# Kernel optimization log

Hardware: AMD Instinct MI355X
Metric: run time of the kernel (lower is better)

Reference implementation:

```python
import jax, jax.numpy as jnp
import numpy as np
import math

N_HEADS = 16
EMBED_DIM = 1024
HEAD_DIM = EMBED_DIM // N_HEADS


def setup_inputs() -> dict:
    key = jax.random.key(0)
    k1, k2, k3 = jax.random.split(key, 3)
    bs, seq_len = 2, 2048
    x = jax.random.normal(k1, (bs, seq_len, EMBED_DIM), dtype=jnp.float32)
    # torch Linear weights are [out_features, in_features]
    W_in = jax.random.normal(k2, (3 * EMBED_DIM, EMBED_DIM), dtype=jnp.float32) * (1.0 / math.sqrt(EMBED_DIM))
    W_out = jax.random.normal(k3, (EMBED_DIM, EMBED_DIM), dtype=jnp.float32) * (1.0 / math.sqrt(EMBED_DIM))
    return {"x": x, "W_in": W_in, "W_out": W_out, "casual_mask": 1}


def reference(x, W_in, W_out, casual_mask):
    bs, seq_len, embed_dim = x.shape
    # fused QKV projection: x @ W_in.T -> [bs, seq, 3E]
    qkv = jnp.einsum('bse,fe->bsf', x, W_in)
    q, k, v = jnp.split(qkv, 3, axis=-1)
    # [bs, heads, seq, head_dim]
    def to_heads(t):
        return t.reshape(bs, seq_len, N_HEADS, HEAD_DIM).transpose(0, 2, 1, 3)
    q, k, v = to_heads(q), to_heads(k), to_heads(v)
    score = jnp.einsum('bhqd,bhkd->bhqk', q, k)
    if casual_mask:  # static Python flag
        causal = jnp.triu(jnp.ones((seq_len, seq_len), dtype=bool), k=1)
        score = jnp.where(causal, -jnp.inf, score)
    score = score / jnp.asarray(math.sqrt(HEAD_DIM), dtype=score.dtype)
    attn = jax.nn.softmax(score, axis=-1)
    out = jnp.einsum('bhqk,bhkd->bhqd', attn, v)
    out = out.transpose(0, 2, 1, 3).reshape(bs, seq_len, embed_dim)
    return jnp.einsum('bse,fe->bsf', out, W_out)
```

## Files before the change

### kernel.cpp

```cpp
#include <hip/hip_runtime.h>
#include <stdint.h>

#define SEQ 2048
#define BS 2
#define EMB 1024
#define NH 16
#define HD 64
#define F3 3072

using f32x4 = __attribute__((ext_vector_type(4))) float;
using bf16x8 = __attribute__((ext_vector_type(8))) short;

__device__ __forceinline__ unsigned short f2bf(float f) {
    union { float f; uint32_t u; } v; v.f = f;
    uint32_t u = v.u;
    u = u + 0x7FFFu + ((u >> 16) & 1u);
    return (unsigned short)(u >> 16);
}

__device__ __forceinline__ uint32_t pk_bf16(float a, float b) {
    uint32_t r;
    asm("v_cvt_pk_bf16_f32 %0, %1, %2" : "=v"(r) : "v"(a), "v"(b));
    return r;
}

#define GLOAD_LDS16(g, l) \
    __builtin_amdgcn_global_load_lds((const __attribute__((address_space(1))) void*)(g), \
                                     (__attribute__((address_space(3))) void*)(l), 16, 0, 0)

__global__ void cvt_kernel(const float* __restrict__ in, unsigned short* __restrict__ out, int n4) {
    int i = blockIdx.x * blockDim.x + threadIdx.x;
    if (i < n4) {
        f32x4 v = reinterpret_cast<const f32x4*>(in)[i];
        uint2 o;
        o.x = pk_bf16(v.x, v.y);
        o.y = pk_bf16(v.z, v.w);
        reinterpret_cast<uint2*>(out)[i] = o;
    }
}

template <bool BF16OUT>
__global__ __launch_bounds__(256) void gemm_bt(
    const unsigned short* __restrict__ A,
    const unsigned short* __restrict__ B,
    void* __restrict__ Cv,
    int M, int N, int K, int nbx)
{
    __shared__ unsigned short As[128 * 32];
    __shared__ unsigned short Bs[128 * 32];
    const int tid  = threadIdx.x;
    const int wave = tid >> 6, lane = tid & 63;
    const int wr = wave >> 1, wc = wave & 1;

    const int nwg = gridDim.x;
    const int s = (blockIdx.x & 7) * (nwg >> 3) + (blockIdx.x >> 3);
    const int bx = s % nbx, by = s / nbx;
    const int row0 = by * 128, col0 = bx * 128;

    f32x4 acc[4][4] = {};

    const int srow = wave * 16 + (lane >> 2);
    const int scol = (lane & 3) * 8;

    const unsigned short* gA = A + (size_t)(row0 + srow) * K + scol;
    const unsigned short* gB = B + (size_t)(col0 + srow) * K + scol;
    unsigned short* lA = As + wave * 16 * 32;
    unsigned short* lB = Bs + wave * 16 * 32;

    for (int kb = 0; kb < K; kb += 32) {
        __syncthreads();
        GLOAD_LDS16(gA + kb,                    lA);
        GLOAD_LDS16(gA + (size_t)64 * K + kb,   lA + 64 * 32);
        GLOAD_LDS16(gB + kb,                    lB);
        GLOAD_LDS16(gB + (size_t)64 * K + kb,   lB + 64 * 32);
        asm volatile("s_waitcnt vmcnt(0)" ::: "memory");
        __syncthreads();

        bf16x8 af[4], bfr[4];
#pragma unroll
        for (int mi = 0; mi < 4; mi++)
            af[mi] = *reinterpret_cast<const bf16x8*>(As + (wr * 64 + mi * 16 + (lane & 15)) * 32 + (lane >> 4) * 8);
#pragma unroll
        for (int ni = 0; ni < 4; ni++)
            bfr[ni] = *reinterpret_cast<const bf16x8*>(Bs + (wc * 64 + ni * 16 + (lane & 15)) * 32 + (lane >> 4) * 8);
#pragma unroll
        for (int mi = 0; mi < 4; mi++)
#pragma unroll
            for (int ni = 0; ni < 4; ni++)
                acc[mi][ni] = __builtin_amdgcn_mfma_f32_16x16x32_bf16(af[mi], bfr[ni], acc[mi][ni], 0, 0, 0);
    }

#pragma unroll
    for (int mi = 0; mi < 4; mi++)
#pragma unroll
        for (int ni = 0; ni < 4; ni++)
#pragma unroll
            for (int r = 0; r < 4; r++) {
                int row = row0 + wr * 64 + mi * 16 + (lane >> 4) * 4 + r;
                int col = col0 + wc * 64 + ni * 16 + (lane & 15);
                float v = acc[mi][ni][r];
                if constexpr (BF16OUT)
                    ((unsigned short*)Cv)[(size_t)row * N + col] = f2bf(v);
                else
                    ((float*)Cv)[(size_t)row * N + col] = v;
            }
}

__global__ __launch_bounds__(256) void attn_kernel(
    const unsigned short* __restrict__ qkv,
    unsigned short* __restrict__ ao)
{
    const int idx = blockIdx.x;
    const int qb = 15 - (idx >> 5);
    const int bh = idx & 31;
    const int b = bh >> 4, h = bh & 15;
    const int tid = threadIdx.x, wave = tid >> 6, lane = tid & 63;
    const int c = lane & 15, g = lane >> 4;

    __shared__ unsigned short Ks[64 * 64];
    __shared__ unsigned short Vs[64 * 64];
    __shared__ unsigned short Ps[4][32 * 64];

    const size_t base = (size_t)b * SEQ * F3;
    const int qrow0 = qb * 128 + wave * 32;
    const float SC = 0.18033688011f;

    bf16x8 qf[2][2];
#pragma unroll
    for (int qt = 0; qt < 2; qt++)
#pragma unroll
        for (int sdq = 0; sdq < 2; sdq++) {
            int row = qrow0 + qt * 16 + c;
            int d   = sdq * 32 + g * 8;
            qf[qt][sdq] = *reinterpret_cast<const bf16x8*>(qkv + base + (size_t)row * F3 + h * HD + d);
        }

    f32x4 po[2][4] = {};
    float mR[2], lR[2];
    mR[0] = mR[1] = -1e30f; lR[0] = lR[1] = 0.f;

    const int ktiles = (qb * 128 + 128) >> 6;
    const int ksrow = tid >> 3;
    const int sch   = tid & 7;
    const int krow2 = (tid >> 3) * 2;

    const unsigned short* gK = qkv + base + EMB     + h * HD + sch * 8;
    const unsigned short* gV = qkv + base + 2 * EMB + h * HD + sch * 8;

    bf16x8 kp0 = *reinterpret_cast<const bf16x8*>(gK + (size_t)ksrow * F3);
    bf16x8 kp1 = *reinterpret_cast<const bf16x8*>(gK + (size_t)(32 + ksrow) * F3);
    bf16x8 vp0 = *reinterpret_cast<const bf16x8*>(gV + (size_t)krow2 * F3);
    bf16x8 vp1 = *reinterpret_cast<const bf16x8*>(gV + (size_t)(krow2 + 1) * F3);

    for (int kt_i = 0; kt_i < ktiles; kt_i++) {
        const int kbase = kt_i * 64;
        __syncthreads();
        {
            int off0 = (ksrow * 128 + sch * 16) ^ ((ksrow & 7) << 4);
            *reinterpret_cast<bf16x8*>((char*)Ks + off0) = kp0;
            int r1 = 32 + ksrow;
            int off1 = (r1 * 128 + sch * 16) ^ ((r1 & 7) << 4);
            *reinterpret_cast<bf16x8*>((char*)Ks + off1) = kp1;
        }
#pragma unroll
        for (int j = 0; j < 8; j++) {
            int d = sch * 8 + j;
            int off = (d * 128 + krow2 * 2) ^ ((((d & 7) ^ (d >> 3)) & 7) << 4);
            ushort2 pr; pr.x = (unsigned short)vp0[j]; pr.y = (unsigned short)vp1[j];
            *reinterpret_cast<ushort2*>((char*)Vs + off) = pr;
        }
        __syncthreads();

        if (kt_i + 1 < ktiles) {
            const int nb = kbase + 64;
            kp0 = *reinterpret_cast<const bf16x8*>(gK + (size_t)(nb + ksrow) * F3);
            kp1 = *reinterpret_cast<const bf16x8*>(gK + (size_t)(nb + 32 + ksrow) * F3);
            vp0 = *reinterpret_cast<const bf16x8*>(gV + (size_t)(nb + krow2) * F3);
            vp1 = *reinterpret_cast<const bf16x8*>(gV + (size_t)(nb + krow2 + 1) * F3);
        }

        const bool active = kbase <= qrow0 + 31;
        if (active) {
            f32x4 st[4][2] = {};
#pragma unroll
            for (int dstep = 0; dstep < 2; dstep++) {
                bf16x8 kf[4];
#pragma unroll
                for (int kt = 0; kt < 4; kt++) {
                    int row = kt * 16 + c;
                    int off = (row * 128 + dstep * 64 + g * 16) ^ ((row & 7) << 4);
                    kf[kt] = *reinterpret_cast<const bf16x8*>((char*)Ks + off);
                }
#pragma unroll
                for (int kt = 0; kt < 4; kt++)
#pragma unroll
                    for (int qt = 0; qt < 2; qt++)
                        st[kt][qt] = __builtin_amdgcn_mfma_f32_16x16x32_bf16(kf[kt], qf[qt][dstep], st[kt][qt], 0, 0, 0);
            }

            const bool needmask = (kbase + 63) > qrow0;
#pragma unroll
            for (int qt = 0; qt < 2; qt++) {
                const int q = qrow0 + qt * 16 + c;
                float mx = -3.0e38f;
#pragma unroll
                for (int kt = 0; kt < 4; kt++)
#pragma unroll
                    for (int r = 0; r < 4; r++) {
                        float v = st[kt][qt][r];
                        if (needmask) {
                            int k = kbase + kt * 16 + g * 4 + r;
                            if (k > q) v = -3.0e38f;
                        }
                        st[kt][qt][r] = v;
                        mx = fmaxf(mx, v);
                    }
                mx = fmaxf(mx, __shfl_xor(mx, 16));
                mx = fmaxf(mx, __shfl_xor(mx, 32));

                const bool skip = __all(mx - mR[qt] <= 8.0f);
                float mn = skip ? mR[qt] : fmaxf(mR[qt], mx);
                const float nmn = -mn * SC;
                float rs = 0.f;
#pragma unroll
                for (int kt = 0; kt < 4; kt++)
#pragma unroll
                    for (int r = 0; r < 4; r++) {
                        float p = __builtin_amdgcn_exp2f(__builtin_fmaf(st[kt][qt][r], SC, nmn));
                        st[kt][qt][r] = p;
                        rs += p;
                    }
                rs += __shfl_xor(rs, 16);
                rs += __shfl_xor(rs, 32);
                if (skip) {
                    lR[qt] += rs;
                } else {
                    float alpha = __builtin_amdgcn_exp2f((mR[qt] - mn) * SC);
                    mR[qt] = mn;
                    lR[qt] = lR[qt] * alpha + rs;
#pragma unroll
                    for (int r = 0; r < 4; r++) {
                        float ar = __shfl(alpha, (g << 2) + r);
#pragma unroll
                        for (int ni = 0; ni < 4; ni++) po[qt][ni][r] *= ar;
                    }
                }
            }

            unsigned short* Pw = Ps[wave];
#pragma unroll
            for (int qt = 0; qt < 2; qt++) {
                int row = qt * 16 + c;
#pragma unroll
                for (int kt = 0; kt < 4; kt++) {
                    uint2 pk;
                    pk.x = pk_bf16(st[kt][qt][0], st[kt][qt][1]);
                    pk.y = pk_bf16(st[kt][qt][2], st[kt][qt][3]);
                    int off = (row * 128 + kt * 32 + g * 8) ^ ((row & 7) << 4);
                    *reinterpret_cast<uint2*>((char*)Pw + off) = pk;
                }
            }

#pragma unroll
            for (int s2 = 0; s2 < 2; s2++) {
                bf16x8 pa[2], vb[4];
#pragma unroll
                for (int mi = 0; mi < 2; mi++) {
                    int row = mi * 16 + c;
                    int off = (row * 128 + s2 * 64 + g * 16) ^ ((row & 7) << 4);
                    pa[mi] = *reinterpret_cast<const bf16x8*>((char*)Pw + off);
                }
#pragma unroll
                for (int ni = 0; ni < 4; ni++) {
                    int n = ni * 16 + c;
                    int off = (n * 128 + s2 * 64 + g * 16) ^ ((((n & 7) ^ (n >> 3)) & 7) << 4);
                    vb[ni] = *reinterpret_cast<const bf16x8*>((char*)Vs + off);
                }
#pragma unroll
                for (int mi = 0; mi < 2; mi++)
#pragma unroll
                    for (int ni = 0; ni < 4; ni++)
                        po[mi][ni] = __builtin_amdgcn_mfma_f32_16x16x32_bf16(pa[mi], vb[ni], po[mi][ni], 0, 0, 0);
            }
        }
    }

#pragma unroll
    for (int qt = 0; qt < 2; qt++) {
        float invl = 1.0f / lR[qt];
#pragma unroll
        for (int r = 0; r < 4; r++) {
            float iv = __shfl(invl, (g << 2) + r);
            int row = qrow0 + qt * 16 + g * 4 + r;
#pragma unroll
            for (int ni = 0; ni < 4; ni++) {
                int d = ni * 16 + c;
                ao[(size_t)(b * SEQ + row) * EMB + h * HD + d] = f2bf(po[qt][ni][r] * iv);
            }
        }
    }
}

extern "C" void kernel_launch(void* const* d_in, const int* in_sizes, int n_in,
                              void* d_out, int out_size, void* d_ws, size_t ws_size,
                              hipStream_t stream)
{
    const float* x    = (const float*)d_in[0];
    const float* Win  = (const float*)d_in[1];
    const float* Wout = (const float*)d_in[2];
    float* out = (float*)d_out;

    char* ws = (char*)d_ws;
    unsigned short* xb    = (unsigned short*)(ws);
    unsigned short* winb  = (unsigned short*)(ws + (8u  << 20));
    unsigned short* woutb = (unsigned short*)(ws + (14u << 20));
    unsigned short* qkvb  = (unsigned short*)(ws + (16u << 20));
    unsigned short* aob   = (unsigned short*)(ws + (40u << 20));

    const int nx    = BS * SEQ * EMB;
    const int nwin  = F3 * EMB;
    const int nwout = EMB * EMB;

    cvt_kernel<<<nx    / 4 / 256, 256, 0, stream>>>(x,    xb,    nx / 4);
    cvt_kernel<<<nwin  / 4 / 256, 256, 0, stream>>>(Win,  winb,  nwin / 4);
    cvt_kernel<<<nwout / 4 / 256, 256, 0, stream>>>(Wout, woutb, nwout / 4);

    gemm_bt<true><<<dim3(768), 256, 0, stream>>>(xb, winb, (void*)qkvb, BS * SEQ, F3, EMB, F3 / 128);

    attn_kernel<<<dim3(512), 256, 0, stream>>>(qkvb, aob);

    gemm_bt<false><<<dim3(256), 256, 0, stream>>>(aob, woutb, (void*)out, BS * SEQ, EMB, EMB, EMB / 128);
}
```

Baseline: 205.9 us.

## Halve attention query tile to 64 rows and remap block scheduling

Each attention block now handles 64 query rows (16 per wave) instead of 128, doubling the grid to 1024 blocks and remapping block indices so heavy causal q-blocks launch first across interleaved heads. This improves occupancy, load balance and reduces wasted masked work per wave, and lowers register use. The cost is halved reuse of each K/V tile loaded into shared memory, increasing global and LDS traffic per query.

Result: faster. 191.6 us (-6.9%).

```diff
diff --git a/kernel.cpp b/kernel.cpp
--- a/kernel.cpp
+++ b/kernel.cpp
@@ -110,36 +110,34 @@
     const unsigned short* __restrict__ qkv,
     unsigned short* __restrict__ ao)
 {
-    const int idx = blockIdx.x;
-    const int qb = 15 - (idx >> 5);
-    const int bh = idx & 31;
+    const int o = blockIdx.x;
+    const int pos = o >> 3;
+    const int bh = (o & 7) * 4 + (pos & 3);
+    const int qb = 31 - (pos >> 2);
     const int b = bh >> 4, h = bh & 15;
     const int tid = threadIdx.x, wave = tid >> 6, lane = tid & 63;
     const int c = lane & 15, g = lane >> 4;
 
     __shared__ unsigned short Ks[64 * 64];
     __shared__ unsigned short Vs[64 * 64];
-    __shared__ unsigned short Ps[4][32 * 64];
+    __shared__ unsigned short Ps[4][16 * 64];
 
     const size_t base = (size_t)b * SEQ * F3;
-    const int qrow0 = qb * 128 + wave * 32;
+    const int qrow0 = qb * 64 + wave * 16;
     const float SC = 0.18033688011f;
 
-    bf16x8 qf[2][2];
-#pragma unroll
-    for (int qt = 0; qt < 2; qt++)
-#pragma unroll
-        for (int sdq = 0; sdq < 2; sdq++) {
-            int row = qrow0 + qt * 16 + c;
-            int d   = sdq * 32 + g * 8;
-            qf[qt][sdq] = *reinterpret_cast<const bf16x8*>(qkv + base + (size_t)row * F3 + h * HD + d);
-        }
-
-    f32x4 po[2][4] = {};
-    float mR[2], lR[2];
-    mR[0] = mR[1] = -1e30f; lR[0] = lR[1] = 0.f;
-
-    const int ktiles = (qb * 128 + 128) >> 6;
+    bf16x8 qf[2];
+#pragma unroll
+    for (int sdq = 0; sdq < 2; sdq++) {
+        int row = qrow0 + c;
+        int d   = sdq * 32 + g * 8;
+        qf[sdq] = *reinterpret_cast<const bf16x8*>(qkv + base + (size_t)row * F3 + h * HD + d);
+    }
+
+    f32x4 po[4] = {};
+    float mR = -1e30f, lR = 0.f;
+
+    const int ktiles = qb + 1;
     const int ksrow = tid >> 3;
     const int sch   = tid & 7;
     const int krow2 = (tid >> 3) * 2;
@@ -179,123 +177,112 @@
             vp1 = *reinterpret_cast<const bf16x8*>(gV + (size_t)(nb + krow2 + 1) * F3);
         }
 
-        const bool active = kbase <= qrow0 + 31;
-        if (active) {
-            f32x4 st[4][2] = {};
-#pragma unroll
-            for (int dstep = 0; dstep < 2; dstep++) {
-                bf16x8 kf[4];
-#pragma unroll
-                for (int kt = 0; kt < 4; kt++) {
-                    int row = kt * 16 + c;
-                    int off = (row * 128 + dstep * 64 + g * 16) ^ ((row & 7) << 4);
-                    kf[kt] = *reinterpret_cast<const bf16x8*>((char*)Ks + off);
+        f32x4 st[4] = {};
+#pragma unroll
+        for (int dstep = 0; dstep < 2; dstep++) {
+            bf16x8 kf[4];
+#pragma unroll
+            for (int kt = 0; kt < 4; kt++) {
+                int row = kt * 16 + c;
+                int off = (row * 128 + dstep * 64 + g * 16) ^ ((row & 7) << 4);
+                kf[kt] = *reinterpret_cast<const bf16x8*>((char*)Ks + off);
+            }
+#pragma unroll
+            for (int kt = 0; kt < 4; kt++)
+                st[kt] = __builtin_amdgcn_mfma_f32_16x16x32_bf16(kf[kt], qf[dstep], st[kt], 0, 0, 0);
+        }
+
+        const bool needmask = (kt_i == qb);
+        {
+            const int q = qrow0 + c;
+            float mx = -3.0e38f;
+#pragma unroll
+            for (int kt = 0; kt < 4; kt++)
+#pragma unroll
+                for (int r = 0; r < 4; r++) {
+                    float v = st[kt][r];
+                    if (needmask) {
+                        int k = kbase + kt * 16 + g * 4 + r;
+                        if (k > q) v = -3.0e38f;
+                    }
+                    st[kt][r] = v;
+                    mx = fmaxf(mx, v);
                 }
-#pragma unroll
-                for (int kt = 0; kt < 4; kt++)
-#pragma unroll
-                    for (int qt = 0; qt < 2; qt++)
-                        st[kt][qt] = __builtin_amdgcn_mfma_f32_16x16x32_bf16(kf[kt], qf[qt][dstep], st[kt][qt], 0, 0, 0);
-            }
-
-            const bool needmask = (kbase + 63) > qrow0;
-#pragma unroll
-            for (int qt = 0; qt < 2; qt++) {
-                const int q = qrow0 + qt * 16 + c;
-                float mx = -3.0e38f;
-#pragma unroll
-                for (int kt = 0; kt < 4; kt++)
-#pragma unroll
-                    for (int r = 0; r < 4; r++) {
-                        float v = st[kt][qt][r];
-                        if (needmask) {
-                            int k = kbase + kt * 16 + g * 4 + r;
-                            if (k > q) v = -3.0e38f;
-                        }
-                        st[kt][qt][r] = v;
-                        mx = fmaxf(mx, v);
-                    }
-                mx = fmaxf(mx, __shfl_xor(mx, 16));
-                mx = fmaxf(mx, __shfl_xor(mx, 32));
-
-                const bool skip = __all(mx - mR[qt] <= 8.0f);
-                float mn = skip ? mR[qt] : fmaxf(mR[qt], mx);
-                const float nmn = -mn * SC;
-                float rs = 0.f;
-#pragma unroll
-                for (int kt = 0; kt < 4; kt++)
-#pragma unroll
-                    for (int r = 0; r < 4; r++) {
-                        float p = __builtin_amdgcn_exp2f(__builtin_fmaf(st[kt][qt][r], SC, nmn));
-                        st[kt][qt][r] = p;
-                        rs += p;
-                    }
-                rs += __shfl_xor(rs, 16);
-                rs += __shfl_xor(rs, 32);
-                if (skip) {
-                    lR[qt] += rs;
-                } else {
-                    float alpha = __builtin_amdgcn_exp2f((mR[qt] - mn) * SC);
-                    mR[qt] = mn;
-                    lR[qt] = lR[qt] * alpha + rs;
-#pragma unroll
-                    for (int r = 0; r < 4; r++) {
-                        float ar = __shfl(alpha, (g << 2) + r);
-#pragma unroll
-                        for (int ni = 0; ni < 4; ni++) po[qt][ni][r] *= ar;
-                    }
+            mx = fmaxf(mx, __shfl_xor(mx, 16));
+            mx = fmaxf(mx, __shfl_xor(mx, 32));
+
+            const bool skip = __all(mx - mR <= 8.0f);
+            float mn = skip ? mR : fmaxf(mR, mx);
+            const float nmn = -mn * SC;
+            float rs = 0.f;
+#pragma unroll
+            for (int kt = 0; kt < 4; kt++)
+#pragma unroll
+                for (int r = 0; r < 4; r++) {
+                    float p = __builtin_amdgcn_exp2f(__builtin_fmaf(st[kt][r], SC, nmn));
+                    st[kt][r] = p;
+                    rs += p;
                 }
-            }
-
-            unsigned short* Pw = Ps[wave];
-#pragma unroll
-            for (int qt = 0; qt < 2; qt++) {
-                int row = qt * 16 + c;
-#pragma unroll
-                for (int kt = 0; kt < 4; kt++) {
-                    uint2 pk;
-                    pk.x = pk_bf16(st[kt][qt][0], st[kt][qt][1]);
-                    pk.y = pk_bf16(st[kt][qt][2], st[kt][qt][3]);
-                    int off = (row * 128 + kt * 32 + g * 8) ^ ((row & 7) << 4);
-                    *reinterpret_cast<uint2*>((char*)Pw + off) = pk;
+            rs += __shfl_xor(rs, 16);
+            rs += __shfl_xor(rs, 32);
+            if (skip) {
+                lR += rs;
+            } else {
+                float alpha = __builtin_amdgcn_exp2f((mR - mn) * SC);
+                mR = mn;
+                lR = lR * alpha + rs;
+#pragma unroll
+                for (int r = 0; r < 4; r++) {
+                    float ar = __shfl(alpha, (g << 2) + r);
+#pragma unroll
+                    for (int ni = 0; ni < 4; ni++) po[ni][r] *= ar;
                 }
             }
-
-#pragma unroll
-            for (int s2 = 0; s2 < 2; s2++) {
-                bf16x8 pa[2], vb[4];
-#pragma unroll
-                for (int mi = 0; mi < 2; mi++) {
-                    int row = mi * 16 + c;
-                    int off = (row * 128 + s2 * 64 + g * 16) ^ ((row & 7) << 4);
-                    pa[mi] = *reinterpret_cast<const bf16x8*>((char*)Pw + off);
-                }
-#pragma unroll
-                for (int ni = 0; ni < 4; ni++) {
-                    int n = ni * 16 + c;
-                    int off = (n * 128 + s2 * 64 + g * 16) ^ ((((n & 7) ^ (n >> 3)) & 7) << 4);
-                    vb[ni] = *reinterpret_cast<const bf16x8*>((char*)Vs + off);
-                }
-#pragma unroll
-                for (int mi = 0; mi < 2; mi++)
-#pragma unroll
-                    for (int ni = 0; ni < 4; ni++)
-                        po[mi][ni] = __builtin_amdgcn_mfma_f32_16x16x32_bf16(pa[mi], vb[ni], po[mi][ni], 0, 0, 0);
-            }
-        }
-    }
-
-#pragma unroll
-    for (int qt = 0; qt < 2; qt++) {
-        float invl = 1.0f / lR[qt];
+        }
+
+        unsigned short* Pw = Ps[wave];
+        {
+            int row = c;
+#pragma unroll
+            for (int kt = 0; kt < 4; kt++) {
+                uint2 pk;
+                pk.x = pk_bf16(st[kt][0], st[kt][1]);
+                pk.y = pk_bf16(st[kt][2], st[kt][3]);
+                int off = (row * 128 + kt * 32 + g * 8) ^ ((row & 7) << 4);
+                *reinterpret_cast<uint2*>((char*)Pw + off) = pk;
+            }
+        }
+
+#pragma unroll
+        for (int s2 = 0; s2 < 2; s2++) {
+            bf16x8 pa, vb[4];
+            {
+                int row = c;
+                int off = (row * 128 + s2 * 64 + g * 16) ^ ((row & 7) << 4);
+                pa = *reinterpret_cast<const bf16x8*>((char*)Pw + off);
+            }
+#pragma unroll
+            for (int ni = 0; ni < 4; ni++) {
+                int n = ni * 16 + c;
+                int off = (n * 128 + s2 * 64 + g * 16) ^ ((((n & 7) ^ (n >> 3)) & 7) << 4);
+                vb[ni] = *reinterpret_cast<const bf16x8*>((char*)Vs + off);
+            }
+#pragma unroll
+            for (int ni = 0; ni < 4; ni++)
+                po[ni] = __builtin_amdgcn_mfma_f32_16x16x32_bf16(pa, vb[ni], po[ni], 0, 0, 0);
+        }
+    }
+
+    {
+        float invl = 1.0f / lR;
 #pragma unroll
         for (int r = 0; r < 4; r++) {
             float iv = __shfl(invl, (g << 2) + r);
-            int row = qrow0 + qt * 16 + g * 4 + r;
+            int row = qrow0 + g * 4 + r;
 #pragma unroll
             for (int ni = 0; ni < 4; ni++) {
                 int d = ni * 16 + c;
-                ao[(size_t)(b * SEQ + row) * EMB + h * HD + d] = f2bf(po[qt][ni][r] * iv);
+                ao[(size_t)(b * SEQ + row) * EMB + h * HD + d] = f2bf(po[ni][r] * iv);
             }
         }
     }
@@ -327,7 +314,7 @@
 
     gemm_bt<true><<<dim3(768), 256, 0, stream>>>(xb, winb, (void*)qkvb, BS * SEQ, F3, EMB, F3 / 128);
 
-    attn_kernel<<<dim3(512), 256, 0, stream>>>(qkvb, aob);
+    attn_kernel<<<dim3(1024), 256, 0, stream>>>(qkvb, aob);
 
     gemm_bt<false><<<dim3(256), 256, 0, stream>>>(aob, woutb, (void*)out, BS * SEQ, EMB, EMB, EMB / 128);
 }
```
